# Kernel tuning notes

Hardware: AMD Instinct MI355X
Metric: run time of the kernel (lower is better)

The kernel has to match this reference:

```python
import jax, jax.numpy as jnp
import numpy as np

B, L, D, K, NRBF = 2, 2048, 128, 3, 16
NUM_ATOMS = 118


def setup_inputs() -> dict:
    key = jax.random.key(0)
    ks = jax.random.split(key, 20)
    s = 0.05
    inp = {
        "coords": jax.random.normal(ks[0], (B, L, 3), dtype=jnp.float32) * 3.0,
        "Z": jax.random.randint(ks[1], (B, L), 0, NUM_ATOMS),
        # CoordEncoder params
        "atom_emb": jax.random.normal(ks[2], (NUM_ATOMS, D), dtype=jnp.float32) * s,
        "gamma": jnp.asarray(10.0, dtype=jnp.float32),
        "rbf_centers": jnp.linspace(0.0, 5.0, NRBF, dtype=jnp.float32),
        "rbf_w": jax.random.normal(ks[3], (NRBF, D), dtype=jnp.float32) * s,
        "rbf_b": jnp.zeros((D,), dtype=jnp.float32),
        "out_w": jax.random.normal(ks[4], (2 * D, D), dtype=jnp.float32) * s,
        "out_b": jnp.zeros((D,), dtype=jnp.float32),
        # MP_Layer params, stacked over K layers
        "self_w": jax.random.normal(ks[5], (K, D, D), dtype=jnp.float32) * s,
        "self_b": jnp.zeros((K, D), dtype=jnp.float32),
        "msg_w": jax.random.normal(ks[6], (K, D, D), dtype=jnp.float32) * s,
        "msg_b": jnp.zeros((K, D), dtype=jnp.float32),
        "upd_w": jax.random.normal(ks[7], (K, 2 * D, D), dtype=jnp.float32) * s,
        "upd_b": jnp.zeros((K, D), dtype=jnp.float32),
    }
    return inp


def _pairwise_dist(coords):
    # coords: [B,L,3] -> dist: [B,L,L]; safe sqrt so diagonal has zero grad
    diff = coords[:, :, None, :] - coords[:, None, :, :]
    sq = jnp.sum(diff * diff, axis=-1)
    return jnp.where(sq > 0, jnp.sqrt(jnp.where(sq > 0, sq, 1.0)), 0.0)


def reference(coords, Z, atom_emb, gamma, rbf_centers, rbf_w, rbf_b,
              out_w, out_b, self_w, self_b, msg_w, msg_b, upd_w, upd_b):
    # --- CoordEncoder ---
    h_atom = atom_emb[Z]                                   # [B,L,D]
    dist = _pairwise_dist(coords)                          # [B,L,L]
    rbf = jnp.exp(-gamma * (dist[..., None] - rbf_centers) ** 2)  # [B,L,L,R]
    rbf_local = rbf.mean(axis=2)                           # [B,L,R]
    h_geo = rbf_local @ rbf_w + rbf_b                      # [B,L,D]
    h = jnp.concatenate([h_atom, h_geo], axis=-1) @ out_w + out_b  # [B,L,D]
    # --- MP layers (mask is None; W = exp(-dist) is the same every layer) ---
    W = jnp.exp(-dist)                                     # [B,L,L]
    for k in range(K):
        msg = jnp.einsum("bij,bjd->bid", W, h @ msg_w[k] + msg_b[k])
        h = jnp.concatenate([h @ self_w[k] + self_b[k], msg], axis=-1) @ upd_w[k] + upd_b[k]
    return h
```

## Files before the change

### kernel.cpp

```cpp
#include <hip/hip_runtime.h>
#include <hip/hip_bf16.h>

typedef unsigned short u16;
typedef __bf16 bf16x8 __attribute__((ext_vector_type(8)));
typedef float f32x4 __attribute__((ext_vector_type(4)));
typedef u16 u16x4 __attribute__((ext_vector_type(4)));

#define B_ 2
#define L_ 2048
#define D_ 128
#define KLAY 3
#define NR 16
#define DD (D_ * D_)
#define XTN (L_ * D_)
#define BL (B_ * L_)
#define BLN (BL * NR)
#define NFOLD 6

static __device__ __forceinline__ u16 f2bf(float f) {
    union { float f; unsigned u; } v; v.f = f;
    unsigned r = v.u + 0x7FFFu + ((v.u >> 16) & 1u);
    return (u16)(r >> 16);
}
static __device__ __forceinline__ bf16x8 ld_bf8(const u16* p) {
    return *(const bf16x8*)p;
}

__global__ __launch_bounds__(512) void pairw_kernel(
    const float* coords, const float* gamma_p, const float* centers,
    const float* self_w, const float* msg_w, const float* upd_w,
    const float* self_b, const float* msg_b, const float* upd_b,
    float* rbfp, float* rsp, u16* foldA, u16* foldB, float* c0v, float* cvv) {
    int bid = blockIdx.x;
    int tid = threadIdx.x;
    __shared__ __align__(16) char smem[34816];
    f32x4 z = {0.f, 0.f, 0.f, 0.f};

    if (bid < NFOLD) {
        int w = tid >> 6, lane = tid & 63;
        int rowf = lane & 15, kg = lane >> 4;
        int lay = bid >> 1, mat = bid & 1;
        const float* Wsrc = (mat ? msg_w : self_w) + lay * DD;
        const float* U = upd_w + lay * 2 * DD + mat * DD;
        u16* dst = (mat ? foldB : foldA) + lay * DD;
        u16(*A_l)[68] = (u16(*)[68])smem;
        u16(*BT_l)[68] = (u16(*)[68])(smem + 17408);
        f32x4 acc[8] = {z, z, z, z, z, z, z, z};
        for (int half = 0; half < 2; half++) {
            int m0 = half * 64;
            for (int o = tid; o < 128 * 64; o += 512) {
                int kk = o >> 6, mm = o & 63;
                A_l[kk][mm] = f2bf(Wsrc[kk * D_ + m0 + mm]);
            }
            for (int o = tid; o < 128 * 64; o += 512) {
                int nn = o >> 6, mm = o & 63;
                BT_l[nn][mm] = f2bf(U[(m0 + mm) * D_ + nn]);
            }
            __syncthreads();
#pragma unroll
            for (int rf = 0; rf < 8; rf++)
#pragma unroll
                for (int ks = 0; ks < 2; ks++) {
                    int k0 = ks * 32 + kg * 8;
                    acc[rf] = __builtin_amdgcn_mfma_f32_16x16x32_bf16(
                        ld_bf8(&A_l[rf * 16 + rowf][k0]),
                        ld_bf8(&BT_l[w * 16 + rowf][k0]), acc[rf], 0, 0, 0);
                }
            __syncthreads();
        }
        int n = w * 16 + rowf;
#pragma unroll
        for (int rf = 0; rf < 8; rf++) {
            u16x4 pk;
#pragma unroll
            for (int r = 0; r < 4; r++) pk[r] = f2bf(acc[rf][r]);
            *(u16x4*)&dst[n * D_ + rf * 16 + kg * 4] = pk;
        }
        if (tid < D_) {
            const float* bsrc = (mat ? msg_b : self_b) + lay * D_;
            float s = 0.f;
            for (int m = 0; m < D_; m++) s += bsrc[m] * U[m * D_ + tid];
            if (mat == 0) c0v[lay * D_ + tid] = s + upd_b[lay * D_ + tid];
            else cvv[lay * D_ + tid] = s;
        }
        return;
    }

    int rt = (bid - NFOLD) >> 2, jq = (bid - NFOLD) & 3;
    int gi0 = rt * 16;
    int b = gi0 >> 11;
    int row = tid >> 5, s5 = tid & 31;
    int gi = gi0 + row;
    float* cj = (float*)smem;
    {
        const float4* src = (const float4*)(coords + ((size_t)b * L_ + jq * 512) * 3);
        if (tid < 384) ((float4*)cj)[tid] = src[tid];
    }
    float gamma = gamma_p[0];
    float dl = centers[1] - centers[0];
    float c4[4];
#pragma unroll
    for (int g = 0; g < 4; g++) c4[g] = centers[4 * g];
    float two_gdl = 2.f * gamma * dl;
    float cx = coords[gi * 3 + 0];
    float cy = coords[gi * 3 + 1];
    float cz = coords[gi * 3 + 2];
    __syncthreads();

    float acc[4][4];
#pragma unroll
    for (int g = 0; g < 4; g++)
#pragma unroll
        for (int m = 0; m < 4; m++) acc[g][m] = 0.f;
    float wsum = 0.f;
#pragma unroll 4
    for (int it = 0; it < 16; it++) {
        int jl = s5 + 32 * it;
        float dx = cx - cj[jl * 3 + 0];
        float dy = cy - cj[jl * 3 + 1];
        float dz = cz - cj[jl * 3 + 2];
        float sq = dx * dx + dy * dy + dz * dz;
        float d = sqrtf(sq);
        wsum += __expf(-d);
#pragma unroll
        for (int g = 0; g < 4; g++) {
            float x = d - c4[g];
            float base = __expf(-gamma * x * x);
            float u1 = __expf(fminf(two_gdl * x, 29.f));
            float u2 = u1 * u1;
            acc[g][0] += base;
            acc[g][1] += base * u1;
            acc[g][2] += base * u2;
            acc[g][3] += base * (u2 * u1);
        }
    }
#pragma unroll
    for (int off = 16; off > 0; off >>= 1) {
        wsum += __shfl_xor(wsum, off);
#pragma unroll
        for (int g = 0; g < 4; g++)
#pragma unroll
            for (int m = 0; m < 4; m++) acc[g][m] += __shfl_xor(acc[g][m], off);
    }
    if (s5 == 0) {
        rsp[(size_t)jq * BL + gi] = wsum;
#pragma unroll
        for (int m = 0; m < 4; m++) {
            float Km = __expf(-gamma * (m * dl) * (m * dl)) * (1.0f / L_);
#pragma unroll
            for (int g = 0; g < 4; g++)
                rbfp[(size_t)jq * BLN + (size_t)gi * NR + 4 * g + m] = acc[g][m] * Km;
        }
    }
}

__global__ __launch_bounds__(256) void encf_kernel(
    const int* Z, const float* atom_emb, const float* rbf_w, const float* rbf_b,
    const float* out_w, const float* out_b, const float* rbfp, const float* rsp,
    u16* h_rm, u16* hT, float* rowsum) {
    int gi0 = blockIdx.x * 16;
    int b = gi0 >> 11;
    int il0 = gi0 & (L_ - 1);
    int tid = threadIdx.x;
    int w = tid >> 6, lane = tid & 63;
    int rowf = lane & 15, kg = lane >> 4;
    __shared__ float rbf_lds[16][NR];
    __shared__ __align__(16) u16 hgeo[16][136];

    {
        int row = tid >> 4, r = tid & 15;
        float s = 0.f;
#pragma unroll
        for (int p = 0; p < 4; p++)
            s += rbfp[(size_t)p * BLN + (size_t)(gi0 + row) * NR + r];
        rbf_lds[row][r] = s;
    }
    if (tid < 16) {
        float s = 0.f;
#pragma unroll
        for (int p = 0; p < 4; p++) s += rsp[(size_t)p * BL + gi0 + tid];
        rowsum[gi0 + tid] = s;
    }
    __syncthreads();
    for (int e = tid; e < 16 * D_; e += 256) {
        int row = e >> 7, d = e & 127;
        float s = rbf_b[d];
#pragma unroll
        for (int r = 0; r < NR; r++) s += rbf_lds[row][r] * rbf_w[r * D_ + d];
        hgeo[row][d] = f2bf(s);
    }
    __syncthreads();

    f32x4 z = {0.f, 0.f, 0.f, 0.f};
    int za = Z[gi0 + rowf];
#pragma unroll
    for (int q = 0; q < 2; q++) {
        int cl = (w * 2 + q) * 16 + rowf;
        f32x4 a1 = z;
#pragma unroll
        for (int ks = 0; ks < 8; ks++) {
            int k0 = ks * 32 + kg * 8;
            bf16x8 av;
            if (k0 < 128) {
                union { bf16x8 v; u16 e[8]; } t;
                const float* ap = atom_emb + (size_t)za * D_ + k0;
#pragma unroll
                for (int e = 0; e < 8; e++) t.e[e] = f2bf(ap[e]);
                av = t.v;
            } else {
                av = ld_bf8(&hgeo[rowf][k0 - 128]);
            }
            union { bf16x8 v; u16 e[8]; } bv;
            const float* bp = out_w + (size_t)k0 * D_ + cl;
#pragma unroll
            for (int e = 0; e < 8; e++) bv.e[e] = f2bf(bp[e * D_]);
            a1 = __builtin_amdgcn_mfma_f32_16x16x32_bf16(av, bv.v, a1, 0, 0, 0);
        }
        float bias = out_b[cl];
        u16x4 pk;
#pragma unroll
        for (int r = 0; r < 4; r++) pk[r] = f2bf(a1[r] + bias);
#pragma unroll
        for (int r = 0; r < 4; r++)
            h_rm[(size_t)(gi0 + kg * 4 + r) * D_ + cl] = pk[r];
        int jj = il0 + kg * 4;
        *(u16x4*)&hT[(size_t)b * XTN + (jj >> 5) * (32 * D_) + cl * 32 + (jj & 31)] = pk;
    }
}

__global__ __launch_bounds__(1024) void mp_kernel(
    const float* coords, const u16* h_in, const u16* hT_in, const float* rowsum,
    const u16* foldA_k, const u16* foldB_k, const float* c0_k, const float* cv_k,
    u16* h_out, u16* hT_out, float* out_f32, int last) {
    int rt = blockIdx.x;
    int gi0 = rt * 16;
    int b = gi0 >> 11;
    int il0 = gi0 & (L_ - 1);
    int tid = threadIdx.x;
    int w = tid >> 6, lane = tid & 63;
    int rowf = lane & 15, kg = lane >> 4;

    __shared__ __align__(16) float cj[L_ * 3];
    __shared__ __align__(16) float red[4][16][128];
    u16* g_lds = (u16*)&red[0][0][0];

    for (int i = tid; i < 1536; i += 1024)
        ((float4*)cj)[i] = ((const float4*)(coords + (size_t)b * L_ * 3))[i];
    __syncthreads();

    float rx = cj[(il0 + rowf) * 3 + 0];
    float ry = cj[(il0 + rowf) * 3 + 1];
    float rz = cj[(il0 + rowf) * 3 + 2];

    f32x4 z = {0.f, 0.f, 0.f, 0.f};
    f32x4 acc[8] = {z, z, z, z, z, z, z, z};
    const u16* xbase = hT_in + (size_t)b * XTN + (w * 4) * (32 * D_) + rowf * 32 + kg * 8;
#pragma unroll
    for (int s = 0; s < 4; s++) {
        int j0 = w * 128 + s * 32 + kg * 8;
        union { bf16x8 v; __bf16 e[8]; } wf;
#pragma unroll
        for (int e = 0; e < 8; e++) {
            int jl = j0 + e;
            float dx = rx - cj[jl * 3 + 0];
            float dy = ry - cj[jl * 3 + 1];
            float dz = rz - cj[jl * 3 + 2];
            float sq = dx * dx + dy * dy + dz * dz;
            float d = sq > 0.f ? sqrtf(sq) : 0.f;
            wf.e[e] = (__bf16)__expf(-d);
        }
#pragma unroll
        for (int n = 0; n < 8; n++) {
            bf16x8 bb = ld_bf8(xbase + s * (32 * D_) + n * 512);
            acc[n] = __builtin_amdgcn_mfma_f32_16x16x32_bf16(wf.v, bb, acc[n], 0, 0, 0);
        }
    }
    auto stash = [&](int slot) {
#pragma unroll
        for (int n = 0; n < 8; n++)
#pragma unroll
            for (int r = 0; r < 4; r++) {
                int row = kg * 4 + r, col = n * 16 + rowf;
                red[slot][row][(col + 4 * row) & 127] = acc[n][r];
            }
    };
    auto grab = [&](int slot) {
#pragma unroll
        for (int n = 0; n < 8; n++)
#pragma unroll
            for (int r = 0; r < 4; r++) {
                int row = kg * 4 + r, col = n * 16 + rowf;
                acc[n][r] += red[slot][row][(col + 4 * row) & 127];
            }
    };
    if (w >= 8 && w < 12) stash(w - 8);
    __syncthreads();
    if (w < 4) grab(w);
    __syncthreads();
    if (w >= 12) stash(w - 12);
    __syncthreads();
    if (w >= 4 && w < 8) grab(w - 4);
    __syncthreads();
    if (w >= 4 && w < 8) stash(w - 4);
    __syncthreads();
    if (w < 4) grab(w);
    if (w == 2 || w == 3) stash(w);
    __syncthreads();
    if (w < 2) grab(w + 2);
    if (w == 1) stash(3);
    __syncthreads();
    if (w == 0) {
        grab(3);
#pragma unroll
        for (int n = 0; n < 8; n++)
#pragma unroll
            for (int r = 0; r < 4; r++)
                g_lds[(kg * 4 + r) * 136 + n * 16 + rowf] = f2bf(acc[n][r]);
    }
    __syncthreads();

    if (w < 8) {
        f32x4 acc2 = z;
        int cl = w * 16 + rowf;
#pragma unroll
        for (int ks = 0; ks < 4; ks++) {
            int k0 = ks * 32 + kg * 8;
            bf16x8 ah = ld_bf8(h_in + (size_t)(gi0 + rowf) * D_ + k0);
            acc2 = __builtin_amdgcn_mfma_f32_16x16x32_bf16(
                ah, ld_bf8(foldA_k + cl * D_ + k0), acc2, 0, 0, 0);
            bf16x8 ag = ld_bf8(g_lds + rowf * 136 + k0);
            acc2 = __builtin_amdgcn_mfma_f32_16x16x32_bf16(
                ag, ld_bf8(foldB_k + cl * D_ + k0), acc2, 0, 0, 0);
        }
        float c0 = c0_k[cl], cv = cv_k[cl];
        if (last) {
#pragma unroll
            for (int r = 0; r < 4; r++) {
                int row = kg * 4 + r;
                out_f32[(size_t)(gi0 + row) * D_ + cl] =
                    acc2[r] + c0 + rowsum[gi0 + row] * cv;
            }
        } else {
#pragma unroll
            for (int r = 0; r < 4; r++) {
                int row = kg * 4 + r;
                float val = acc2[r] + c0 + rowsum[gi0 + row] * cv;
                u16 hv = f2bf(val);
                h_out[(size_t)(gi0 + row) * D_ + cl] = hv;
                int jj = il0 + row;
                hT_out[(size_t)b * XTN + (jj >> 5) * (32 * D_) + cl * 32 + (jj & 31)] = hv;
            }
        }
    }
}

extern "C" void kernel_launch(void* const* d_in, const int* in_sizes, int n_in,
                              void* d_out, int out_size, void* d_ws, size_t ws_size,
                              hipStream_t stream) {
    const float* coords = (const float*)d_in[0];
    const int* Z = (const int*)d_in[1];
    const float* atom_emb = (const float*)d_in[2];
    const float* gamma = (const float*)d_in[3];
    const float* centers = (const float*)d_in[4];
    const float* rbf_w = (const float*)d_in[5];
    const float* rbf_b = (const float*)d_in[6];
    const float* out_w = (const float*)d_in[7];
    const float* out_b = (const float*)d_in[8];
    const float* self_w = (const float*)d_in[9];
    const float* self_b = (const float*)d_in[10];
    const float* msg_w = (const float*)d_in[11];
    const float* msg_b = (const float*)d_in[12];
    const float* upd_w = (const float*)d_in[13];
    const float* upd_b = (const float*)d_in[14];
    float* out = (float*)d_out;

    char* ws = (char*)d_ws;
    u16* h_a = (u16*)(ws + 0);
    u16* h_b = (u16*)(ws + 1048576);
    u16* hT_a = (u16*)(ws + 2097152);
    u16* hT_b = (u16*)(ws + 3145728);
    float* rowsum = (float*)(ws + 4194304);
    u16* foldA = (u16*)(ws + 4210688);
    u16* foldB = (u16*)(ws + 4308992);
    float* c0v = (float*)(ws + 4407296);
    float* cvv = (float*)(ws + 4408832);
    float* rbfp = (float*)(ws + 4410368);
    float* rsp = (float*)(ws + 5458944);

    pairw_kernel<<<NFOLD + 1024, 512, 0, stream>>>(
        coords, gamma, centers, self_w, msg_w, upd_w, self_b, msg_b, upd_b,
        rbfp, rsp, foldA, foldB, c0v, cvv);
    encf_kernel<<<256, 256, 0, stream>>>(
        Z, atom_emb, rbf_w, rbf_b, out_w, out_b, rbfp, rsp, h_a, hT_a, rowsum);
    mp_kernel<<<256, 1024, 0, stream>>>(
        coords, h_a, hT_a, rowsum, foldA + 0 * DD, foldB + 0 * DD,
        c0v + 0 * D_, cvv + 0 * D_, h_b, hT_b, out, 0);
    mp_kernel<<<256, 1024, 0, stream>>>(
        coords, h_b, hT_b, rowsum, foldA + 1 * DD, foldB + 1 * DD,
        c0v + 1 * D_, cvv + 1 * D_, h_a, hT_a, out, 0);
    mp_kernel<<<256, 1024, 0, stream>>>(
        coords, h_a, hT_a, rowsum, foldA + 2 * DD, foldB + 2 * DD,
        c0v + 2 * D_, cvv + 2 * D_, h_b, hT_b, out, 1);
}
```

Baseline: 98.27 us.

## Precompute bf16 exp(-dist) matrix once and stream it into MP layers

The pairwise kernel now writes exp(-d) as bf16 into a global matrix laid out in MFMA fragment order. The message-passing kernels load that matrix instead of recomputing distances and exponentials from coordinates in every layer. The MP kernel's split over waves changes: each wave owns one 16-column output tile and half the j range, so the long multi-stage LDS reduction becomes a single two-way reduction. The cost is a 16 MB write plus three full reads of W per layer, which trades ALU work for memory bandwidth.

```diff
diff --git a/kernel.cpp b/kernel.cpp
--- a/kernel.cpp
+++ b/kernel.cpp
@@ -30,7 +30,8 @@
     const float* coords, const float* gamma_p, const float* centers,
     const float* self_w, const float* msg_w, const float* upd_w,
     const float* self_b, const float* msg_b, const float* upd_b,
-    float* rbfp, float* rsp, u16* foldA, u16* foldB, float* c0v, float* cvv) {
+    float* rbfp, float* rsp, u16* Wf,
+    u16* foldA, u16* foldB, float* c0v, float* cvv) {
     int bid = blockIdx.x;
     int tid = threadIdx.x;
     __shared__ __align__(16) char smem[34816];
@@ -86,11 +87,12 @@
         return;
     }
 
-    int rt = (bid - NFOLD) >> 2, jq = (bid - NFOLD) & 3;
+    int e6 = bid - NFOLD;
+    int rt = e6 >> 2, jq = e6 & 3;
     int gi0 = rt * 16;
     int b = gi0 >> 11;
-    int row = tid >> 5, s5 = tid & 31;
-    int gi = gi0 + row;
+    int prow = tid >> 5, s5 = tid & 31;
+    int gi = gi0 + prow;
     float* cj = (float*)smem;
     {
         const float4* src = (const float4*)(coords + ((size_t)b * L_ + jq * 512) * 3);
@@ -113,6 +115,7 @@
 #pragma unroll
         for (int m = 0; m < 4; m++) acc[g][m] = 0.f;
     float wsum = 0.f;
+    u16* wst = Wf + (size_t)rt * (64 * 512) + (size_t)jq * 16 * 512 + tid;
 #pragma unroll 4
     for (int it = 0; it < 16; it++) {
         int jl = s5 + 32 * it;
@@ -121,7 +124,9 @@
         float dz = cz - cj[jl * 3 + 2];
         float sq = dx * dx + dy * dy + dz * dz;
         float d = sqrtf(sq);
-        wsum += __expf(-d);
+        float ex = __expf(-d);
+        wsum += ex;
+        wst[it * 512] = f2bf(ex);
 #pragma unroll
         for (int g = 0; g < 4; g++) {
             float x = d - c4[g];
@@ -229,7 +234,7 @@
 }
 
 __global__ __launch_bounds__(1024) void mp_kernel(
-    const float* coords, const u16* h_in, const u16* hT_in, const float* rowsum,
+    const u16* Wf, const u16* h_in, const u16* hT_in, const float* rowsum,
     const u16* foldA_k, const u16* foldB_k, const float* c0_k, const float* cv_k,
     u16* h_out, u16* hT_out, float* out_f32, int last) {
     int rt = blockIdx.x;
@@ -239,83 +244,32 @@
     int tid = threadIdx.x;
     int w = tid >> 6, lane = tid & 63;
     int rowf = lane & 15, kg = lane >> 4;
-
-    __shared__ __align__(16) float cj[L_ * 3];
-    __shared__ __align__(16) float red[4][16][128];
-    u16* g_lds = (u16*)&red[0][0][0];
-
-    for (int i = tid; i < 1536; i += 1024)
-        ((float4*)cj)[i] = ((const float4*)(coords + (size_t)b * L_ * 3))[i];
-    __syncthreads();
-
-    float rx = cj[(il0 + rowf) * 3 + 0];
-    float ry = cj[(il0 + rowf) * 3 + 1];
-    float rz = cj[(il0 + rowf) * 3 + 2];
+    int nb = w & 7, jh = w >> 3;
+
+    __shared__ float red[8][16][20];
+    __shared__ __align__(16) u16 g_lds[16][136];
 
     f32x4 z = {0.f, 0.f, 0.f, 0.f};
-    f32x4 acc[8] = {z, z, z, z, z, z, z, z};
-    const u16* xbase = hT_in + (size_t)b * XTN + (w * 4) * (32 * D_) + rowf * 32 + kg * 8;
-#pragma unroll
-    for (int s = 0; s < 4; s++) {
-        int j0 = w * 128 + s * 32 + kg * 8;
-        union { bf16x8 v; __bf16 e[8]; } wf;
-#pragma unroll
-        for (int e = 0; e < 8; e++) {
-            int jl = j0 + e;
-            float dx = rx - cj[jl * 3 + 0];
-            float dy = ry - cj[jl * 3 + 1];
-            float dz = rz - cj[jl * 3 + 2];
-            float sq = dx * dx + dy * dy + dz * dz;
-            float d = sq > 0.f ? sqrtf(sq) : 0.f;
-            wf.e[e] = (__bf16)__expf(-d);
-        }
-#pragma unroll
-        for (int n = 0; n < 8; n++) {
-            bf16x8 bb = ld_bf8(xbase + s * (32 * D_) + n * 512);
-            acc[n] = __builtin_amdgcn_mfma_f32_16x16x32_bf16(wf.v, bb, acc[n], 0, 0, 0);
-        }
-    }
-    auto stash = [&](int slot) {
-#pragma unroll
-        for (int n = 0; n < 8; n++)
-#pragma unroll
-            for (int r = 0; r < 4; r++) {
-                int row = kg * 4 + r, col = n * 16 + rowf;
-                red[slot][row][(col + 4 * row) & 127] = acc[n][r];
-            }
-    };
-    auto grab = [&](int slot) {
-#pragma unroll
-        for (int n = 0; n < 8; n++)
-#pragma unroll
-            for (int r = 0; r < 4; r++) {
-                int row = kg * 4 + r, col = n * 16 + rowf;
-                acc[n][r] += red[slot][row][(col + 4 * row) & 127];
-            }
-    };
-    if (w >= 8 && w < 12) stash(w - 8);
-    __syncthreads();
-    if (w < 4) grab(w);
-    __syncthreads();
-    if (w >= 12) stash(w - 12);
-    __syncthreads();
-    if (w >= 4 && w < 8) grab(w - 4);
-    __syncthreads();
-    if (w >= 4 && w < 8) stash(w - 4);
-    __syncthreads();
-    if (w < 4) grab(w);
-    if (w == 2 || w == 3) stash(w);
-    __syncthreads();
-    if (w < 2) grab(w + 2);
-    if (w == 1) stash(3);
-    __syncthreads();
-    if (w == 0) {
-        grab(3);
-#pragma unroll
-        for (int n = 0; n < 8; n++)
-#pragma unroll
-            for (int r = 0; r < 4; r++)
-                g_lds[(kg * 4 + r) * 136 + n * 16 + rowf] = f2bf(acc[n][r]);
+    f32x4 acc = z;
+    const u16* abase = Wf + (size_t)rt * (64 * 512) + (size_t)jh * 32 * 512 +
+                       rowf * 32 + kg * 8;
+    const u16* xbase = hT_in + (size_t)b * XTN + (size_t)jh * 32 * (32 * D_) +
+                       (nb * 16 + rowf) * 32 + kg * 8;
+#pragma unroll 4
+    for (int s = 0; s < 32; s++) {
+        bf16x8 a = ld_bf8(abase + s * 512);
+        bf16x8 bb = ld_bf8(xbase + (size_t)s * (32 * D_));
+        acc = __builtin_amdgcn_mfma_f32_16x16x32_bf16(a, bb, acc, 0, 0, 0);
+    }
+    if (jh == 1) {
+#pragma unroll
+        for (int r = 0; r < 4; r++) red[nb][kg * 4 + r][rowf] = acc[r];
+    }
+    __syncthreads();
+    if (jh == 0) {
+#pragma unroll
+        for (int r = 0; r < 4; r++)
+            g_lds[kg * 4 + r][nb * 16 + rowf] = f2bf(acc[r] + red[nb][kg * 4 + r][rowf]);
     }
     __syncthreads();
 
@@ -328,7 +282,7 @@
             bf16x8 ah = ld_bf8(h_in + (size_t)(gi0 + rowf) * D_ + k0);
             acc2 = __builtin_amdgcn_mfma_f32_16x16x32_bf16(
                 ah, ld_bf8(foldA_k + cl * D_ + k0), acc2, 0, 0, 0);
-            bf16x8 ag = ld_bf8(g_lds + rowf * 136 + k0);
+            bf16x8 ag = ld_bf8(&g_lds[rowf][k0]);
             acc2 = __builtin_amdgcn_mfma_f32_16x16x32_bf16(
                 ag, ld_bf8(foldB_k + cl * D_ + k0), acc2, 0, 0, 0);
         }
@@ -386,19 +340,20 @@
     float* cvv = (float*)(ws + 4408832);
     float* rbfp = (float*)(ws + 4410368);
     float* rsp = (float*)(ws + 5458944);
+    u16* Wf = (u16*)(ws + 5524480);
 
     pairw_kernel<<<NFOLD + 1024, 512, 0, stream>>>(
         coords, gamma, centers, self_w, msg_w, upd_w, self_b, msg_b, upd_b,
-        rbfp, rsp, foldA, foldB, c0v, cvv);
+        rbfp, rsp, Wf, foldA, foldB, c0v, cvv);
     encf_kernel<<<256, 256, 0, stream>>>(
         Z, atom_emb, rbf_w, rbf_b, out_w, out_b, rbfp, rsp, h_a, hT_a, rowsum);
     mp_kernel<<<256, 1024, 0, stream>>>(
-        coords, h_a, hT_a, rowsum, foldA + 0 * DD, foldB + 0 * DD,
+        Wf, h_a, hT_a, rowsum, foldA + 0 * DD, foldB + 0 * DD,
         c0v + 0 * D_, cvv + 0 * D_, h_b, hT_b, out, 0);
     mp_kernel<<<256, 1024, 0, stream>>>(
-        coords, h_b, hT_b, rowsum, foldA + 1 * DD, foldB + 1 * DD,
+        Wf, h_b, hT_b, rowsum, foldA + 1 * DD, foldB + 1 * DD,
         c0v + 1 * D_, cvv + 1 * D_, h_a, hT_a, out, 0);
     mp_kernel<<<256, 1024, 0, stream>>>(
-        coords, h_a, hT_a, rowsum, foldA + 2 * DD, foldB + 2 * DD,
+        Wf, h_a, hT_a, rowsum, foldA + 2 * DD, foldB + 2 * DD,
         c0v + 2 * D_, cvv + 2 * D_, h_b, hT_b, out, 1);
 }
```

Result: slower. 107.0 us (+8.8%).
